# Kernel tuning notes

Measured on AMD Instinct MI355X. Metric: run time of the kernel, lower is better.

Reference implementation:

```python
import jax, jax.numpy as jnp
import numpy as np

N, E, F, H, O = 50000, 1_600_000, 512, 256, 128


def setup_inputs() -> dict:
    key = jax.random.key(0)
    k1, k2, k3, k4, k5 = jax.random.split(key, 5)
    x = jax.random.normal(k1, (N, F), dtype=jnp.float32)
    edge_index = jax.random.randint(k2, (2, E), 0, N, dtype=jnp.int32)
    edge_weight = jax.random.uniform(k3, (E,), dtype=jnp.float32)
    W1 = jax.random.normal(k4, (F, H), dtype=jnp.float32) * (1.0 / np.sqrt(F))
    b1 = jnp.zeros((H,), dtype=jnp.float32)
    W2 = jax.random.normal(k5, (H, O), dtype=jnp.float32) * (1.0 / np.sqrt(H))
    b2 = jnp.zeros((O,), dtype=jnp.float32)
    return {"x": x, "edge_index": edge_index, "edge_weight": edge_weight,
            "W1": W1, "b1": b1, "W2": W2, "b2": b2}


def reference(x, edge_index, edge_weight, W1, b1, W2, b2):
    n = x.shape[0]
    src, dst = edge_index[0], edge_index[1]
    # GCNConv: add self-loops with weight 1
    loop = jnp.arange(n, dtype=src.dtype)
    src = jnp.concatenate([src, loop])
    dst = jnp.concatenate([dst, loop])
    w = jnp.concatenate([edge_weight, jnp.ones((n,), dtype=x.dtype)])
    # symmetric normalization D^{-1/2} (A+I) D^{-1/2}
    deg = jax.ops.segment_sum(w, dst, num_segments=n)
    dinv = jnp.where(deg > 0, jax.lax.rsqrt(deg), 0.0)
    norm = dinv[src] * w * dinv[dst]  # [E+N]

    def conv(h, W, b):
        h = h @ W                                   # linear first (PyG GCNConv)
        msg = h[src] * norm[:, None]                # gather + scale per edge
        return jax.ops.segment_sum(msg, dst, num_segments=n) + b

    h = jax.nn.relu(conv(x, W1, b1))
    return conv(h, W2, b2)
```

## Files before the change

### kernel.cpp

```cpp
#include <hip/hip_runtime.h>
#include <hip/hip_bf16.h>

#define CAP 80
#define NPB 98
#define BCAP 4096
#define CHUNK_E 2048

typedef __attribute__((ext_vector_type(8))) short bf16x8;
typedef __attribute__((ext_vector_type(4))) float f32x4;
typedef __attribute__((ext_vector_type(2))) float f32x2;

__device__ inline ushort f2bf(float f){
  union{float f; unsigned u;} c{f};
  unsigned r = (c.u + 0x7fff + ((c.u>>16)&1)) >> 16;
  return (ushort)r;
}
__device__ inline float blo(unsigned u){ return __uint_as_float(u<<16); }
__device__ inline float bhi(unsigned u){ return __uint_as_float(u & 0xffff0000u); }


__device__ inline unsigned char fp8_enc(float v){
#if __has_builtin(__builtin_amdgcn_cvt_pk_fp8_f32)
  int p = __builtin_amdgcn_cvt_pk_fp8_f32(v, v, 0, false);
  return (unsigned char)(p & 0xff);
#else
  unsigned s = v < 0.f ? 0x80u : 0u;
  float a = fabsf(v);
  if (a >= 448.f) return (unsigned char)(s | 0x7Eu);
  if (a < 7.8125e-3f){
    int m = (int)rintf(a * 512.f); if (m > 15) m = 15;
    if (m >= 8) return (unsigned char)(s | (1u<<3) | (unsigned)(m-8));
    return (unsigned char)(s | (unsigned)m);
  }
  int e; float fr = frexpf(a, &e);
  int m = (int)rintf(fr * 16.f);
  if (m == 16){ m = 8; e++; }
  int ee = e - 1 + 7;
  if (ee > 15) return (unsigned char)(s | 0x7Eu);
  return (unsigned char)(s | (unsigned)(ee<<3) | (unsigned)(m-8));
#endif
}

__device__ inline void fp8x4_dec(unsigned w, float d[4]){
#if __has_builtin(__builtin_amdgcn_cvt_pk_f32_fp8)
  f32x2 lo = __builtin_amdgcn_cvt_pk_f32_fp8((int)w, false);
  f32x2 hi = __builtin_amdgcn_cvt_pk_f32_fp8((int)w, true);
  d[0] = lo[0]; d[1] = lo[1]; d[2] = hi[0]; d[3] = hi[1];
#else
  #pragma unroll
  for (int i = 0; i < 4; ++i){
    unsigned v = (w >> (8*i)) & 0xffu;
    unsigned s = v & 0x80u, e = (v>>3)&15u, m = v&7u;
    float f = e ? ldexpf((float)(8+m), (int)e - 10) : ldexpf((float)m, -9);
    d[i] = s ? -f : f;
  }
#endif
}


__global__ void k_init0(int* a, int n){
  int i = blockIdx.x*blockDim.x + threadIdx.x;
  if (i < n) a[i] = 0;
}


__global__ __launch_bounds__(256) void k_bin(const int* __restrict__ src,
                                             const int* __restrict__ dst,
                                             const float* __restrict__ w,
                                             int* __restrict__ bktcur,
                                             uint2* __restrict__ bkt, int E, int nb){
  __shared__ int hist[512];
  __shared__ int base[512];
  const int t  = threadIdx.x;
  const int c0 = blockIdx.x * CHUNK_E;
  const int cend = min(c0 + CHUNK_E, E);
  for (int i = t; i < nb; i += 256) hist[i] = 0;
  __syncthreads();
  for (int e = c0 + t; e < cend; e += 256)
    atomicAdd(&hist[dst[e]/NPB], 1);
  __syncthreads();
  for (int i = t; i < nb; i += 256){
    int h = hist[i];
    base[i] = (h > 0) ? atomicAdd(&bktcur[i], h) : 0;
    hist[i] = 0;
  }
  __syncthreads();
  for (int e = c0 + t; e < cend; e += 256){
    int d = dst[e];
    int b = d / NPB;
    int pos = base[b] + atomicAdd(&hist[b], 1);
    if (pos < BCAP){
      unsigned lo = ((unsigned)src[e] << 16) | (unsigned)f2bf(w[e]);
      bkt[(size_t)b*BCAP + pos] = make_uint2(lo, (unsigned)d);
    }
  }
}


__global__ __launch_bounds__(256) void k_build(const uint2* __restrict__ bkt,
                                               const int* __restrict__ bktcur,
                                               unsigned* __restrict__ padcsr,
                                               int* __restrict__ cnt,
                                               float* __restrict__ dinv, int N){
  __shared__ unsigned rows[NPB][CAP];
  __shared__ int   lcnt[NPB];
  __shared__ float lws[NPB];
  const int b = blockIdx.x;
  const int t = threadIdx.x;
  const int node0 = b * NPB;
  for (int i = t; i < NPB; i += 256){ lcnt[i] = 0; lws[i] = 0.f; }
  __syncthreads();
  const int cb = min(bktcur[b], BCAP);
  for (int e = t; e < cb; e += 256){
    uint2 rec = bkt[(size_t)b*BCAP + e];
    int ld = (int)rec.y - node0;
    int pos = atomicAdd(&lcnt[ld], 1);
    if (pos < CAP) rows[ld][pos] = rec.x;
    atomicAdd(&lws[ld], blo(rec.x));
  }
  __syncthreads();
  const int maxn = min(NPB, N - node0);
  unsigned* gslice = padcsr + (size_t)node0*CAP;
  const int tot = maxn * CAP;
  const unsigned* lbase = &rows[0][0];
  for (int i = t*4; i < tot; i += 1024)
    *(uint4*)(gslice + i) = *(const uint4*)(lbase + i);
  for (int i = t; i < maxn; i += 256){
    cnt[node0 + i]  = lcnt[i];
    dinv[node0 + i] = rsqrtf(1.f + lws[i]);
  }
}


__global__ __launch_bounds__(256, 2) void gemm1_f8(const float* __restrict__ X,
                                                   const float* __restrict__ Wm,
                                                   unsigned char* __restrict__ out, int M){
  __shared__ short As[128][56];
  __shared__ short Bs[256][56];
  const int t    = threadIdx.x;
  const int lane = t & 63;
  const int wave = t >> 6;
  const int wr   = wave >> 1;
  const int wc   = wave & 1;
  const int i0   = blockIdx.x * 128;

  f32x4 acc[4][8];
  #pragma unroll
  for (int m = 0; m < 4; ++m)
    #pragma unroll
    for (int nn = 0; nn < 8; ++nn)
      acc[m][nn] = (f32x4){0.f,0.f,0.f,0.f};

  const int arow = t >> 1;
  const int akh  = (t & 1) * 16;

  for (int kt = 0; kt < 512; kt += 32){
    {
      int gi = i0 + arow;
      ushort hv[16];
      if (gi < M){
        const float4* ap4 = (const float4*)(X + (size_t)gi*512 + kt + akh);
        #pragma unroll
        for (int q = 0; q < 4; ++q){
          float4 v = ap4[q];
          hv[q*4+0] = f2bf(v.x); hv[q*4+1] = f2bf(v.y);
          hv[q*4+2] = f2bf(v.z); hv[q*4+3] = f2bf(v.w);
        }
      } else {
        #pragma unroll
        for (int q = 0; q < 16; ++q) hv[q] = 0;
      }
      *(uint4*)&As[arow][akh]     = *(uint4*)&hv[0];
      *(uint4*)&As[arow][akh + 8] = *(uint4*)&hv[8];
    }
    {
      #pragma unroll
      for (int s2 = 0; s2 < 4; ++s2){
        int s  = t + s2*256;
        int bn = s & 255;
        int k8 = s >> 8;
        ushort hv[8];
        #pragma unroll
        for (int i = 0; i < 8; ++i){
          float v = Wm[(size_t)(kt + k8*8 + i)*256 + bn];
          hv[i] = f2bf(v);
        }
        *(uint4*)&Bs[bn][k8*8] = *(uint4*)&hv[0];
      }
    }
    __syncthreads();
    bf16x8 a_f[4], b_f[8];
    #pragma unroll
    for (int m = 0; m < 4; ++m)
      a_f[m] = *(bf16x8*)&As[wr*64 + m*16 + (lane & 15)][(lane >> 4) * 8];
    #pragma unroll
    for (int nn = 0; nn < 8; ++nn)
      b_f[nn] = *(bf16x8*)&Bs[wc*128 + nn*16 + (lane & 15)][(lane >> 4) * 8];
    #pragma unroll
    for (int m = 0; m < 4; ++m)
      #pragma unroll
      for (int nn = 0; nn < 8; ++nn)
        acc[m][nn] = __builtin_amdgcn_mfma_f32_16x16x32_bf16(a_f[m], b_f[nn], acc[m][nn], 0, 0, 0);
    __syncthreads();
  }
  #pragma unroll
  for (int m = 0; m < 4; ++m){
    int r_base = i0 + wr*64 + m*16 + ((lane >> 4) << 2);
    #pragma unroll
    for (int nn = 0; nn < 8; ++nn){
      int c = wc*128 + nn*16 + (lane & 15);
      #pragma unroll
      for (int r = 0; r < 4; ++r){
        int gr = r_base + r;
        if (gr < M) out[(size_t)gr*256 + c] = fp8_enc(acc[m][nn][r]);
      }
    }
  }
}


template<typename TIN, int K, int DOUT>
__global__ __launch_bounds__(256) void mfma_gemm(const TIN* __restrict__ X,
                                                 const float* __restrict__ Wm,
                                                 ushort* __restrict__ out, int M){
  __shared__ short As[128][56];
  __shared__ short Bs[128][56];
  const int t    = threadIdx.x;
  const int lane = t & 63;
  const int wave = t >> 6;
  const int wr   = wave >> 1;
  const int wc   = wave & 1;
  const int i0   = blockIdx.x * 128;
  const int n0   = blockIdx.y * 128;

  f32x4 acc[4][4];
  #pragma unroll
  for (int m = 0; m < 4; ++m)
    #pragma unroll
    for (int nn = 0; nn < 4; ++nn)
      acc[m][nn] = (f32x4){0.f,0.f,0.f,0.f};

  const int arow = t >> 1;
  const int akh  = (t & 1) * 16;

  for (int kt = 0; kt < K; kt += 32){
    {
      int gi = i0 + arow;
      ushort hv[16];
      if (gi < M){
        const uint4* ap4 = (const uint4*)(X + (size_t)gi*K + kt + akh);
        uint4 u0 = ap4[0], u1 = ap4[1];
        *(uint4*)&hv[0] = u0; *(uint4*)&hv[8] = u1;
      } else {
        #pragma unroll
        for (int q = 0; q < 16; ++q) hv[q] = 0;
      }
      *(uint4*)&As[arow][akh]     = *(uint4*)&hv[0];
      *(uint4*)&As[arow][akh + 8] = *(uint4*)&hv[8];
    }
    {
      #pragma unroll
      for (int s2 = 0; s2 < 2; ++s2){
        int s  = t + s2*256;
        int bn = s & 127;
        int k8 = s >> 7;
        ushort hv[8];
        #pragma unroll
        for (int i = 0; i < 8; ++i){
          float v = Wm[(size_t)(kt + k8*8 + i)*DOUT + n0 + bn];
          hv[i] = f2bf(v);
        }
        *(uint4*)&Bs[bn][k8*8] = *(uint4*)&hv[0];
      }
    }
    __syncthreads();
    bf16x8 a_f[4], b_f[4];
    #pragma unroll
    for (int m = 0; m < 4; ++m)
      a_f[m] = *(bf16x8*)&As[wr*64 + m*16 + (lane & 15)][(lane >> 4) * 8];
    #pragma unroll
    for (int nn = 0; nn < 4; ++nn)
      b_f[nn] = *(bf16x8*)&Bs[wc*64 + nn*16 + (lane & 15)][(lane >> 4) * 8];
    #pragma unroll
    for (int m = 0; m < 4; ++m)
      #pragma unroll
      for (int nn = 0; nn < 4; ++nn)
        acc[m][nn] = __builtin_amdgcn_mfma_f32_16x16x32_bf16(a_f[m], b_f[nn], acc[m][nn], 0, 0, 0);
    __syncthreads();
  }
  #pragma unroll
  for (int m = 0; m < 4; ++m){
    int r_base = i0 + wr*64 + m*16 + ((lane >> 4) << 2);
    #pragma unroll
    for (int nn = 0; nn < 4; ++nn){
      int c = n0 + wc*64 + nn*16 + (lane & 15);
      #pragma unroll
      for (int r = 0; r < 4; ++r){
        int gr = r_base + r;
        if (gr < M) out[(size_t)gr*DOUT + c] = f2bf(acc[m][nn][r]);
      }
    }
  }
}


__global__ __launch_bounds__(256) void agg_fp8(const unsigned char* __restrict__ tin,
                                               const int* __restrict__ cnt,
                                               const unsigned* __restrict__ padcsr,
                                               const float* __restrict__ dinv,
                                               const float* __restrict__ bias,
                                               ushort* __restrict__ outp, int n){
  constexpr int U = 4;
  int node = blockIdx.x*4 + (threadIdx.x >> 6);
  if (node >= n) return;
  int lane = threadIdx.x & 63;
  int sl   = lane & 15;
  int part = lane >> 4;
  const size_t boff = (size_t)sl * 16;
  const unsigned* row = padcsr + (size_t)node*CAP;

  float acc[16];
  #pragma unroll
  for (int i = 0; i < 16; ++i) acc[i] = 0.f;
  int len = min(cnt[node], CAP);
  int e = 0;
  for (; e + 4*U <= len; e += 4*U){
    int srcs[U]; float ws[U];
    #pragma unroll
    for (int u = 0; u < U; ++u){
      unsigned rec = row[e + u*4 + part];
      srcs[u] = (int)(rec >> 16); ws[u] = blo(rec);
    }
    float dv[U];
    #pragma unroll
    for (int u = 0; u < U; ++u) dv[u] = dinv[srcs[u]];
    uint4 g[U];
    #pragma unroll
    for (int u = 0; u < U; ++u) g[u] = *(const uint4*)(tin + (size_t)srcs[u]*256 + boff);
    #pragma unroll
    for (int u = 0; u < U; ++u){
      float w = ws[u] * dv[u];
      float d[4];
      fp8x4_dec(g[u].x, d);
      acc[0]  += d[0]*w; acc[1]  += d[1]*w; acc[2]  += d[2]*w; acc[3]  += d[3]*w;
      fp8x4_dec(g[u].y, d);
      acc[4]  += d[0]*w; acc[5]  += d[1]*w; acc[6]  += d[2]*w; acc[7]  += d[3]*w;
      fp8x4_dec(g[u].z, d);
      acc[8]  += d[0]*w; acc[9]  += d[1]*w; acc[10] += d[2]*w; acc[11] += d[3]*w;
      fp8x4_dec(g[u].w, d);
      acc[12] += d[0]*w; acc[13] += d[1]*w; acc[14] += d[2]*w; acc[15] += d[3]*w;
    }
  }
  for (; e < len; e += 4){
    int idx = e + part;
    int s = node; float w = 0.f;
    if (idx < len){ unsigned rec = row[idx]; s = (int)(rec >> 16); w = blo(rec) * dinv[s]; }
    uint4 g = *(const uint4*)(tin + (size_t)s*256 + boff);
    float d[4];
    fp8x4_dec(g.x, d);
    acc[0]  += d[0]*w; acc[1]  += d[1]*w; acc[2]  += d[2]*w; acc[3]  += d[3]*w;
    fp8x4_dec(g.y, d);
    acc[4]  += d[0]*w; acc[5]  += d[1]*w; acc[6]  += d[2]*w; acc[7]  += d[3]*w;
    fp8x4_dec(g.z, d);
    acc[8]  += d[0]*w; acc[9]  += d[1]*w; acc[10] += d[2]*w; acc[11] += d[3]*w;
    fp8x4_dec(g.w, d);
    acc[12] += d[0]*w; acc[13] += d[1]*w; acc[14] += d[2]*w; acc[15] += d[3]*w;
  }
  #pragma unroll
  for (int i = 0; i < 16; ++i){
    acc[i] += __shfl_xor(acc[i], 16);
    acc[i] += __shfl_xor(acc[i], 32);
  }
  if (part == 0){
    float di = dinv[node];
    uint4 gs = *(const uint4*)(tin + (size_t)node*256 + boff);
    float d[4];
    fp8x4_dec(gs.x, d);
    acc[0]  += d[0]*di; acc[1]  += d[1]*di; acc[2]  += d[2]*di; acc[3]  += d[3]*di;
    fp8x4_dec(gs.y, d);
    acc[4]  += d[0]*di; acc[5]  += d[1]*di; acc[6]  += d[2]*di; acc[7]  += d[3]*di;
    fp8x4_dec(gs.z, d);
    acc[8]  += d[0]*di; acc[9]  += d[1]*di; acc[10] += d[2]*di; acc[11] += d[3]*di;
    fp8x4_dec(gs.w, d);
    acc[12] += d[0]*di; acc[13] += d[1]*di; acc[14] += d[2]*di; acc[15] += d[3]*di;
    ushort hv[16];
    #pragma unroll
    for (int q = 0; q < 4; ++q){
      float4 bq = *(const float4*)(bias + sl*16 + q*4);
      acc[q*4+0] = acc[q*4+0]*di + bq.x;
      acc[q*4+1] = acc[q*4+1]*di + bq.y;
      acc[q*4+2] = acc[q*4+2]*di + bq.z;
      acc[q*4+3] = acc[q*4+3]*di + bq.w;
    }
    #pragma unroll
    for (int i = 0; i < 16; ++i) hv[i] = f2bf(fmaxf(acc[i], 0.f));
    ushort* op = outp + (size_t)node*256 + sl*16;
    *(uint4*)op       = *(uint4*)&hv[0];
    *(uint4*)(op + 8) = *(uint4*)&hv[8];
  }
}


template<int D, int MODE>
__global__ __launch_bounds__(256) void agg_pad(const ushort* __restrict__ tin,
                                               const int* __restrict__ cnt,
                                               const unsigned* __restrict__ padcsr,
                                               const float* __restrict__ dinv,
                                               const float* __restrict__ bias,
                                               void* __restrict__ outp, int n){
  constexpr int LPR = D/8;
  constexpr int EPW = 64/LPR;
  constexpr int U   = 4;
  int node = blockIdx.x*4 + (threadIdx.x >> 6);
  if (node >= n) return;
  int lane = threadIdx.x & 63;
  int sl   = lane & (LPR-1);
  int part = lane / LPR;
  const size_t boff = (size_t)sl*8;
  const unsigned* row = padcsr + (size_t)node*CAP;

  float acc[8] = {0,0,0,0,0,0,0,0};
  int len = min(cnt[node], CAP);
  int e = 0;
  for (; e + EPW*U <= len; e += EPW*U){
    int srcs[U]; float ws[U];
    #pragma unroll
    for (int u = 0; u < U; ++u){
      unsigned rec = row[e + u*EPW + part];
      srcs[u] = (int)(rec >> 16); ws[u] = blo(rec);
    }
    float dv[U];
    #pragma unroll
    for (int u = 0; u < U; ++u) dv[u] = dinv[srcs[u]];
    uint4 g[U];
    #pragma unroll
    for (int u = 0; u < U; ++u) g[u] = *(const uint4*)(tin + (size_t)srcs[u]*D + boff);
    #pragma unroll
    for (int u = 0; u < U; ++u){
      float w = ws[u] * dv[u];
      acc[0] += blo(g[u].x)*w; acc[1] += bhi(g[u].x)*w;
      acc[2] += blo(g[u].y)*w; acc[3] += bhi(g[u].y)*w;
      acc[4] += blo(g[u].z)*w; acc[5] += bhi(g[u].z)*w;
      acc[6] += blo(g[u].w)*w; acc[7] += bhi(g[u].w)*w;
    }
  }
  for (; e < len; e += EPW){
    int idx = e + part;
    int s = node; float w = 0.f;
    if (idx < len){
      unsigned rec = row[idx];
      s = (int)(rec >> 16);
      w = blo(rec) * dinv[s];
    }
    uint4 g = *(const uint4*)(tin + (size_t)s*D + boff);
    acc[0] += blo(g.x)*w; acc[1] += bhi(g.x)*w;
    acc[2] += blo(g.y)*w; acc[3] += bhi(g.y)*w;
    acc[4] += blo(g.z)*w; acc[5] += bhi(g.z)*w;
    acc[6] += blo(g.w)*w; acc[7] += bhi(g.w)*w;
  }
  #pragma unroll
  for (int i = 0; i < 8; ++i){
    if constexpr (EPW == 4) acc[i] += __shfl_xor(acc[i], 16);
    acc[i] += __shfl_xor(acc[i], 32);
  }
  if (part == 0){
    float di = dinv[node];
    uint4 gs = *(const uint4*)(tin + (size_t)node*D + boff);
    acc[0] += blo(gs.x)*di; acc[1] += bhi(gs.x)*di;
    acc[2] += blo(gs.y)*di; acc[3] += bhi(gs.y)*di;
    acc[4] += blo(gs.z)*di; acc[5] += bhi(gs.z)*di;
    acc[6] += blo(gs.w)*di; acc[7] += bhi(gs.w)*di;
    float4 b0 = *(const float4*)(bias + sl*8);
    float4 b1 = *(const float4*)(bias + sl*8 + 4);
    acc[0] = acc[0]*di + b0.x; acc[1] = acc[1]*di + b0.y;
    acc[2] = acc[2]*di + b0.z; acc[3] = acc[3]*di + b0.w;
    acc[4] = acc[4]*di + b1.x; acc[5] = acc[5]*di + b1.y;
    acc[6] = acc[6]*di + b1.z; acc[7] = acc[7]*di + b1.w;
    if constexpr (MODE == 0){
      ushort hv[8];
      #pragma unroll
      for (int i = 0; i < 8; ++i) hv[i] = f2bf(fmaxf(acc[i], 0.f));
      *(uint4*)((ushort*)outp + (size_t)node*D + boff) = *(uint4*)&hv[0];
    } else {
      float* op = (float*)outp + (size_t)node*D + boff;
      *(float4*)op     = make_float4(acc[0],acc[1],acc[2],acc[3]);
      *(float4*)(op+4) = make_float4(acc[4],acc[5],acc[6],acc[7]);
    }
  }
}


static inline size_t align_up(size_t x){ return (x + 255) & ~(size_t)255; }

extern "C" void kernel_launch(void* const* d_in, const int* in_sizes, int n_in,
                              void* d_out, int out_size, void* d_ws, size_t ws_size,
                              hipStream_t stream){
  const float* x   = (const float*)d_in[0];
  const int*   ei  = (const int*)  d_in[1];
  const float* ew  = (const float*)d_in[2];
  const float* W1  = (const float*)d_in[3];
  const float* b1  = (const float*)d_in[4];
  const float* W2  = (const float*)d_in[5];
  const float* b2  = (const float*)d_in[6];

  const int H = in_sizes[4];
  const int F = in_sizes[3] / H;
  const int N = in_sizes[0] / F;
  const int E = in_sizes[2];

  const int* src = ei;
  const int* dst = ei + E;

  const int nb = (N + NPB - 1) / NPB;

  char* p = (char*)d_ws;
  int*      cnt     = (int*)p;            p += align_up((size_t)N*4);
  float*    dinv    = (float*)p;          p += align_up((size_t)N*4);
  int*      bktcur  = (int*)p;            p += align_up((size_t)nb*4);
  unsigned* padcsr  = (unsigned*)p;       p += align_up((size_t)N*CAP*4);
  unsigned char* t1 = (unsigned char*)p;  p += align_up((size_t)N*H);
  uint2*    bkt     = (uint2*)p;
  ushort*   h1      = (ushort*)p;         p += align_up((size_t)N*H*2 > (size_t)nb*BCAP*8 ?
                                                        (size_t)N*H*2 : (size_t)nb*BCAP*8);
  ushort*   t2      = (ushort*)t1;

  hipLaunchKernelGGL(k_init0, dim3((nb+255)/256), dim3(256), 0, stream, bktcur, nb);
  hipLaunchKernelGGL(k_bin, dim3((E+CHUNK_E-1)/CHUNK_E), dim3(256), 0, stream,
                     src, dst, ew, bktcur, bkt, E, nb);
  hipLaunchKernelGGL(k_build, dim3(nb), dim3(256), 0, stream,
                     bkt, bktcur, padcsr, cnt, dinv, N);

  hipLaunchKernelGGL(gemm1_f8, dim3((N+127)/128), dim3(256), 0, stream, x, W1, t1, N);
  hipLaunchKernelGGL(agg_fp8, dim3((N+3)/4), dim3(256), 0, stream,
                     t1, cnt, padcsr, dinv, b1, h1, N);

  hipLaunchKernelGGL((mfma_gemm<__hip_bfloat16,256,128>), dim3((N+127)/128, 1), dim3(256), 0, stream,
                     (const __hip_bfloat16*)h1, W2, t2, N);
  hipLaunchKernelGGL((agg_pad<128,1>), dim3((N+3)/4), dim3(256), 0, stream,
                     t2, cnt, padcsr, dinv, b2, d_out, N);
}
```

Measured before the change: 242.2 us.

## Split aggregation by feature slice with four threads per node and serial edges

Both aggregation kernels are restructured. A wave no longer handles one node with edges split across lane groups. Each block now covers 64 nodes for one quarter of the feature columns, four threads per node, and each thread walks every edge of its node sequentially. This removes the cross-lane shuffle reduction and the idle lanes in the epilogue, and the feature-slice split is meant to make the gathered rows cache better. In exchange, each thread's edge loop is longer and the CSR row is loaded redundantly by the four slice blocks (as non-temporal loads), with divergence when node degrees differ within a wave.

```diff
diff --git a/kernel.cpp b/kernel.cpp
--- a/kernel.cpp
+++ b/kernel.cpp
@@ -304,189 +304,151 @@
 }
 
 
-__global__ __launch_bounds__(256) void agg_fp8(const unsigned char* __restrict__ tin,
-                                               const int* __restrict__ cnt,
-                                               const unsigned* __restrict__ padcsr,
-                                               const float* __restrict__ dinv,
-                                               const float* __restrict__ bias,
-                                               ushort* __restrict__ outp, int n){
-  constexpr int U = 4;
-  int node = blockIdx.x*4 + (threadIdx.x >> 6);
+__global__ __launch_bounds__(256) void agg1_slice(const unsigned char* __restrict__ tin,
+                                                  const int* __restrict__ cnt,
+                                                  const unsigned* __restrict__ padcsr,
+                                                  const float* __restrict__ dinv,
+                                                  const float* __restrict__ bias,
+                                                  ushort* __restrict__ outp, int n){
+  const int bid   = blockIdx.x;
+  const int slice = bid & 3;
+  const int node  = (bid >> 2)*64 + (threadIdx.x >> 2);
   if (node >= n) return;
-  int lane = threadIdx.x & 63;
-  int sl   = lane & 15;
-  int part = lane >> 4;
-  const size_t boff = (size_t)sl * 16;
+  const int sl = threadIdx.x & 3;
+  const size_t boff = (size_t)slice*64 + sl*16;
   const unsigned* row = padcsr + (size_t)node*CAP;
 
   float acc[16];
   #pragma unroll
   for (int i = 0; i < 16; ++i) acc[i] = 0.f;
-  int len = min(cnt[node], CAP);
+  const int len = min(cnt[node], CAP);
   int e = 0;
-  for (; e + 4*U <= len; e += 4*U){
-    int srcs[U]; float ws[U];
-    #pragma unroll
-    for (int u = 0; u < U; ++u){
-      unsigned rec = row[e + u*4 + part];
-      srcs[u] = (int)(rec >> 16); ws[u] = blo(rec);
-    }
-    float dv[U];
-    #pragma unroll
-    for (int u = 0; u < U; ++u) dv[u] = dinv[srcs[u]];
-    uint4 g[U];
-    #pragma unroll
-    for (int u = 0; u < U; ++u) g[u] = *(const uint4*)(tin + (size_t)srcs[u]*256 + boff);
-    #pragma unroll
-    for (int u = 0; u < U; ++u){
-      float w = ws[u] * dv[u];
+  for (; e + 4 <= len; e += 4){
+    unsigned rec[4];
+    #pragma unroll
+    for (int u = 0; u < 4; ++u) rec[u] = __builtin_nontemporal_load(row + e + u);
+    int   s[4]; float wv[4];
+    #pragma unroll
+    for (int u = 0; u < 4; ++u){ s[u] = (int)(rec[u] >> 16); wv[u] = blo(rec[u]); }
+    float dv[4];
+    #pragma unroll
+    for (int u = 0; u < 4; ++u) dv[u] = dinv[s[u]];
+    uint4 g[4];
+    #pragma unroll
+    for (int u = 0; u < 4; ++u) g[u] = *(const uint4*)(tin + (size_t)s[u]*256 + boff);
+    #pragma unroll
+    for (int u = 0; u < 4; ++u){
+      float w = wv[u]*dv[u];
       float d[4];
-      fp8x4_dec(g[u].x, d);
-      acc[0]  += d[0]*w; acc[1]  += d[1]*w; acc[2]  += d[2]*w; acc[3]  += d[3]*w;
-      fp8x4_dec(g[u].y, d);
-      acc[4]  += d[0]*w; acc[5]  += d[1]*w; acc[6]  += d[2]*w; acc[7]  += d[3]*w;
-      fp8x4_dec(g[u].z, d);
-      acc[8]  += d[0]*w; acc[9]  += d[1]*w; acc[10] += d[2]*w; acc[11] += d[3]*w;
-      fp8x4_dec(g[u].w, d);
-      acc[12] += d[0]*w; acc[13] += d[1]*w; acc[14] += d[2]*w; acc[15] += d[3]*w;
-    }
-  }
-  for (; e < len; e += 4){
-    int idx = e + part;
-    int s = node; float w = 0.f;
-    if (idx < len){ unsigned rec = row[idx]; s = (int)(rec >> 16); w = blo(rec) * dinv[s]; }
+      fp8x4_dec(g[u].x, d); acc[0]+=d[0]*w; acc[1]+=d[1]*w; acc[2]+=d[2]*w; acc[3]+=d[3]*w;
+      fp8x4_dec(g[u].y, d); acc[4]+=d[0]*w; acc[5]+=d[1]*w; acc[6]+=d[2]*w; acc[7]+=d[3]*w;
+      fp8x4_dec(g[u].z, d); acc[8]+=d[0]*w; acc[9]+=d[1]*w; acc[10]+=d[2]*w; acc[11]+=d[3]*w;
+      fp8x4_dec(g[u].w, d); acc[12]+=d[0]*w; acc[13]+=d[1]*w; acc[14]+=d[2]*w; acc[15]+=d[3]*w;
+    }
+  }
+  for (; e < len; ++e){
+    unsigned rec = __builtin_nontemporal_load(row + e);
+    int s = (int)(rec >> 16);
+    float w = blo(rec) * dinv[s];
     uint4 g = *(const uint4*)(tin + (size_t)s*256 + boff);
     float d[4];
-    fp8x4_dec(g.x, d);
-    acc[0]  += d[0]*w; acc[1]  += d[1]*w; acc[2]  += d[2]*w; acc[3]  += d[3]*w;
-    fp8x4_dec(g.y, d);
-    acc[4]  += d[0]*w; acc[5]  += d[1]*w; acc[6]  += d[2]*w; acc[7]  += d[3]*w;
-    fp8x4_dec(g.z, d);
-    acc[8]  += d[0]*w; acc[9]  += d[1]*w; acc[10] += d[2]*w; acc[11] += d[3]*w;
-    fp8x4_dec(g.w, d);
-    acc[12] += d[0]*w; acc[13] += d[1]*w; acc[14] += d[2]*w; acc[15] += d[3]*w;
-  }
-  #pragma unroll
-  for (int i = 0; i < 16; ++i){
-    acc[i] += __shfl_xor(acc[i], 16);
-    acc[i] += __shfl_xor(acc[i], 32);
-  }
-  if (part == 0){
-    float di = dinv[node];
+    fp8x4_dec(g.x, d); acc[0]+=d[0]*w; acc[1]+=d[1]*w; acc[2]+=d[2]*w; acc[3]+=d[3]*w;
+    fp8x4_dec(g.y, d); acc[4]+=d[0]*w; acc[5]+=d[1]*w; acc[6]+=d[2]*w; acc[7]+=d[3]*w;
+    fp8x4_dec(g.z, d); acc[8]+=d[0]*w; acc[9]+=d[1]*w; acc[10]+=d[2]*w; acc[11]+=d[3]*w;
+    fp8x4_dec(g.w, d); acc[12]+=d[0]*w; acc[13]+=d[1]*w; acc[14]+=d[2]*w; acc[15]+=d[3]*w;
+  }
+  const float di = dinv[node];
+  {
     uint4 gs = *(const uint4*)(tin + (size_t)node*256 + boff);
     float d[4];
-    fp8x4_dec(gs.x, d);
-    acc[0]  += d[0]*di; acc[1]  += d[1]*di; acc[2]  += d[2]*di; acc[3]  += d[3]*di;
-    fp8x4_dec(gs.y, d);
-    acc[4]  += d[0]*di; acc[5]  += d[1]*di; acc[6]  += d[2]*di; acc[7]  += d[3]*di;
-    fp8x4_dec(gs.z, d);
-    acc[8]  += d[0]*di; acc[9]  += d[1]*di; acc[10] += d[2]*di; acc[11] += d[3]*di;
-    fp8x4_dec(gs.w, d);
-    acc[12] += d[0]*di; acc[13] += d[1]*di; acc[14] += d[2]*di; acc[15] += d[3]*di;
-    ushort hv[16];
-    #pragma unroll
-    for (int q = 0; q < 4; ++q){
-      float4 bq = *(const float4*)(bias + sl*16 + q*4);
-      acc[q*4+0] = acc[q*4+0]*di + bq.x;
-      acc[q*4+1] = acc[q*4+1]*di + bq.y;
-      acc[q*4+2] = acc[q*4+2]*di + bq.z;
-      acc[q*4+3] = acc[q*4+3]*di + bq.w;
-    }
-    #pragma unroll
-    for (int i = 0; i < 16; ++i) hv[i] = f2bf(fmaxf(acc[i], 0.f));
-    ushort* op = outp + (size_t)node*256 + sl*16;
-    *(uint4*)op       = *(uint4*)&hv[0];
-    *(uint4*)(op + 8) = *(uint4*)&hv[8];
-  }
-}
-
-
-template<int D, int MODE>
-__global__ __launch_bounds__(256) void agg_pad(const ushort* __restrict__ tin,
-                                               const int* __restrict__ cnt,
-                                               const unsigned* __restrict__ padcsr,
-                                               const float* __restrict__ dinv,
-                                               const float* __restrict__ bias,
-                                               void* __restrict__ outp, int n){
-  constexpr int LPR = D/8;
-  constexpr int EPW = 64/LPR;
-  constexpr int U   = 4;
-  int node = blockIdx.x*4 + (threadIdx.x >> 6);
+    fp8x4_dec(gs.x, d); acc[0]+=d[0]*di; acc[1]+=d[1]*di; acc[2]+=d[2]*di; acc[3]+=d[3]*di;
+    fp8x4_dec(gs.y, d); acc[4]+=d[0]*di; acc[5]+=d[1]*di; acc[6]+=d[2]*di; acc[7]+=d[3]*di;
+    fp8x4_dec(gs.z, d); acc[8]+=d[0]*di; acc[9]+=d[1]*di; acc[10]+=d[2]*di; acc[11]+=d[3]*di;
+    fp8x4_dec(gs.w, d); acc[12]+=d[0]*di; acc[13]+=d[1]*di; acc[14]+=d[2]*di; acc[15]+=d[3]*di;
+  }
+  ushort hv[16];
+  #pragma unroll
+  for (int q = 0; q < 4; ++q){
+    float4 bq = *(const float4*)(bias + slice*64 + sl*16 + q*4);
+    acc[q*4+0] = acc[q*4+0]*di + bq.x;
+    acc[q*4+1] = acc[q*4+1]*di + bq.y;
+    acc[q*4+2] = acc[q*4+2]*di + bq.z;
+    acc[q*4+3] = acc[q*4+3]*di + bq.w;
+  }
+  #pragma unroll
+  for (int i = 0; i < 16; ++i) hv[i] = f2bf(fmaxf(acc[i], 0.f));
+  ushort* op = outp + (size_t)node*256 + slice*64 + sl*16;
+  *(uint4*)op       = *(uint4*)&hv[0];
+  *(uint4*)(op + 8) = *(uint4*)&hv[8];
+}
+
+
+__global__ __launch_bounds__(256) void agg2_slice(const ushort* __restrict__ tin,
+                                                  const int* __restrict__ cnt,
+                                                  const unsigned* __restrict__ padcsr,
+                                                  const float* __restrict__ dinv,
+                                                  const float* __restrict__ bias,
+                                                  float* __restrict__ outp, int n){
+  const int bid   = blockIdx.x;
+  const int slice = bid & 3;
+  const int node  = (bid >> 2)*64 + (threadIdx.x >> 2);
   if (node >= n) return;
-  int lane = threadIdx.x & 63;
-  int sl   = lane & (LPR-1);
-  int part = lane / LPR;
-  const size_t boff = (size_t)sl*8;
+  const int sl = threadIdx.x & 3;
+  const size_t eoff = (size_t)slice*32 + sl*8;
   const unsigned* row = padcsr + (size_t)node*CAP;
 
   float acc[8] = {0,0,0,0,0,0,0,0};
-  int len = min(cnt[node], CAP);
+  const int len = min(cnt[node], CAP);
   int e = 0;
-  for (; e + EPW*U <= len; e += EPW*U){
-    int srcs[U]; float ws[U];
-    #pragma unroll
-    for (int u = 0; u < U; ++u){
-      unsigned rec = row[e + u*EPW + part];
-      srcs[u] = (int)(rec >> 16); ws[u] = blo(rec);
-    }
-    float dv[U];
-    #pragma unroll
-    for (int u = 0; u < U; ++u) dv[u] = dinv[srcs[u]];
-    uint4 g[U];
-    #pragma unroll
-    for (int u = 0; u < U; ++u) g[u] = *(const uint4*)(tin + (size_t)srcs[u]*D + boff);
-    #pragma unroll
-    for (int u = 0; u < U; ++u){
-      float w = ws[u] * dv[u];
+  for (; e + 4 <= len; e += 4){
+    unsigned rec[4];
+    #pragma unroll
+    for (int u = 0; u < 4; ++u) rec[u] = __builtin_nontemporal_load(row + e + u);
+    int   s[4]; float wv[4];
+    #pragma unroll
+    for (int u = 0; u < 4; ++u){ s[u] = (int)(rec[u] >> 16); wv[u] = blo(rec[u]); }
+    float dv[4];
+    #pragma unroll
+    for (int u = 0; u < 4; ++u) dv[u] = dinv[s[u]];
+    uint4 g[4];
+    #pragma unroll
+    for (int u = 0; u < 4; ++u) g[u] = *(const uint4*)(tin + (size_t)s[u]*128 + eoff);
+    #pragma unroll
+    for (int u = 0; u < 4; ++u){
+      float w = wv[u]*dv[u];
       acc[0] += blo(g[u].x)*w; acc[1] += bhi(g[u].x)*w;
       acc[2] += blo(g[u].y)*w; acc[3] += bhi(g[u].y)*w;
       acc[4] += blo(g[u].z)*w; acc[5] += bhi(g[u].z)*w;
       acc[6] += blo(g[u].w)*w; acc[7] += bhi(g[u].w)*w;
     }
   }
-  for (; e < len; e += EPW){
-    int idx = e + part;
-    int s = node; float w = 0.f;
-    if (idx < len){
-      unsigned rec = row[idx];
-      s = (int)(rec >> 16);
-      w = blo(rec) * dinv[s];
-    }
-    uint4 g = *(const uint4*)(tin + (size_t)s*D + boff);
+  for (; e < len; ++e){
+    unsigned rec = __builtin_nontemporal_load(row + e);
+    int s = (int)(rec >> 16);
+    float w = blo(rec) * dinv[s];
+    uint4 g = *(const uint4*)(tin + (size_t)s*128 + eoff);
     acc[0] += blo(g.x)*w; acc[1] += bhi(g.x)*w;
     acc[2] += blo(g.y)*w; acc[3] += bhi(g.y)*w;
     acc[4] += blo(g.z)*w; acc[5] += bhi(g.z)*w;
     acc[6] += blo(g.w)*w; acc[7] += bhi(g.w)*w;
   }
-  #pragma unroll
-  for (int i = 0; i < 8; ++i){
-    if constexpr (EPW == 4) acc[i] += __shfl_xor(acc[i], 16);
-    acc[i] += __shfl_xor(acc[i], 32);
-  }
-  if (part == 0){
-    float di = dinv[node];
-    uint4 gs = *(const uint4*)(tin + (size_t)node*D + boff);
+  const float di = dinv[node];
+  {
+    uint4 gs = *(const uint4*)(tin + (size_t)node*128 + eoff);
     acc[0] += blo(gs.x)*di; acc[1] += bhi(gs.x)*di;
     acc[2] += blo(gs.y)*di; acc[3] += bhi(gs.y)*di;
     acc[4] += blo(gs.z)*di; acc[5] += bhi(gs.z)*di;
     acc[6] += blo(gs.w)*di; acc[7] += bhi(gs.w)*di;
-    float4 b0 = *(const float4*)(bias + sl*8);
-    float4 b1 = *(const float4*)(bias + sl*8 + 4);
-    acc[0] = acc[0]*di + b0.x; acc[1] = acc[1]*di + b0.y;
-    acc[2] = acc[2]*di + b0.z; acc[3] = acc[3]*di + b0.w;
-    acc[4] = acc[4]*di + b1.x; acc[5] = acc[5]*di + b1.y;
-    acc[6] = acc[6]*di + b1.z; acc[7] = acc[7]*di + b1.w;
-    if constexpr (MODE == 0){
-      ushort hv[8];
-      #pragma unroll
-      for (int i = 0; i < 8; ++i) hv[i] = f2bf(fmaxf(acc[i], 0.f));
-      *(uint4*)((ushort*)outp + (size_t)node*D + boff) = *(uint4*)&hv[0];
-    } else {
-      float* op = (float*)outp + (size_t)node*D + boff;
-      *(float4*)op     = make_float4(acc[0],acc[1],acc[2],acc[3]);
-      *(float4*)(op+4) = make_float4(acc[4],acc[5],acc[6],acc[7]);
-    }
-  }
+  }
+  float4 b0 = *(const float4*)(bias + slice*32 + sl*8);
+  float4 b1 = *(const float4*)(bias + slice*32 + sl*8 + 4);
+  acc[0] = acc[0]*di + b0.x; acc[1] = acc[1]*di + b0.y;
+  acc[2] = acc[2]*di + b0.z; acc[3] = acc[3]*di + b0.w;
+  acc[4] = acc[4]*di + b1.x; acc[5] = acc[5]*di + b1.y;
+  acc[6] = acc[6]*di + b1.z; acc[7] = acc[7]*di + b1.w;
+  float* op = outp + (size_t)node*128 + slice*32 + sl*8;
+  *(float4*)op     = make_float4(acc[0],acc[1],acc[2],acc[3]);
+  *(float4*)(op+4) = make_float4(acc[4],acc[5],acc[6],acc[7]);
 }
 
 
@@ -530,12 +492,14 @@
   hipLaunchKernelGGL(k_build, dim3(nb), dim3(256), 0, stream,
                      bkt, bktcur, padcsr, cnt, dinv, N);
 
+  const int nodeblocks = (N + 63) / 64;
+
   hipLaunchKernelGGL(gemm1_f8, dim3((N+127)/128), dim3(256), 0, stream, x, W1, t1, N);
-  hipLaunchKernelGGL(agg_fp8, dim3((N+3)/4), dim3(256), 0, stream,
+  hipLaunchKernelGGL(agg1_slice, dim3(nodeblocks*4), dim3(256), 0, stream,
                      t1, cnt, padcsr, dinv, b1, h1, N);
 
   hipLaunchKernelGGL((mfma_gemm<__hip_bfloat16,256,128>), dim3((N+127)/128, 1), dim3(256), 0, stream,
                      (const __hip_bfloat16*)h1, W2, t2, N);
-  hipLaunchKernelGGL((agg_pad<128,1>), dim3((N+3)/4), dim3(256), 0, stream,
-                     t2, cnt, padcsr, dinv, b2, d_out, N);
-}
+  hipLaunchKernelGGL(agg2_slice, dim3(nodeblocks*4), dim3(256), 0, stream,
+                     t2, cnt, padcsr, dinv, b2, (float*)d_out, N);
+}
```

New measurement: 370.1 us. 52.8% more time.
